# Performance work log

Measured on AMD Instinct MI355X. Metric: run time of the kernel, lower is better.

The kernel has to match this reference:

```python
import jax, jax.numpy as jnp
import numpy as np

EPS = 1e-5

def setup_inputs() -> dict:
    key = jax.random.key(0)
    ks = jax.random.split(key, 8)
    B, T, D, S = 8, 4096, 1024, 64
    return {
        "x": jax.random.normal(ks[0], (B, T, D), dtype=jnp.float32),
        "time_decay": jax.random.normal(ks[1], (S,), dtype=jnp.float32) * 0.1 - 0.5,
        "time_first": jax.random.normal(ks[2], (S,), dtype=jnp.float32) * 0.1,
        "W_key": jax.random.normal(ks[3], (S, D), dtype=jnp.float32) * 0.02,
        "W_value": jax.random.normal(ks[4], (S, D), dtype=jnp.float32) * 0.02,
        "W_output": jax.random.normal(ks[5], (D, S), dtype=jnp.float32) * 0.02,
        "W_shift": jax.random.normal(ks[6], (D, D), dtype=jnp.float32) * 0.02,
        "shift_gate": jnp.ones((D,), dtype=jnp.float32),
        "ln_w": jnp.ones((D,), dtype=jnp.float32),
        "ln_b": jnp.zeros((D,), dtype=jnp.float32),
    }


def _forward(x, time_decay, time_first, W_key, W_value, W_output, W_shift, shift_gate, ln_w, ln_b):
    B, T, D = x.shape
    S = time_decay.shape[0]
    # --- token shift: rotate sequence by shift_len, project, gated blend ---
    shift_len = max(1, int(T * 0.5))
    x_cat = jnp.concatenate([x[:, shift_len:], x[:, :-shift_len]], axis=1)  # (B,T,D)
    gate = jax.nn.sigmoid(shift_gate)
    x_shift = jnp.einsum('btd,ed->bte', x_cat, W_shift) * gate + x * (1.0 - gate)
    # --- layernorm (torch: biased variance, eps=1e-5) ---
    mu = jnp.mean(x_shift, axis=-1, keepdims=True)
    var = jnp.mean(jnp.square(x_shift - mu), axis=-1, keepdims=True)
    xn = (x_shift - mu) * jax.lax.rsqrt(var + EPS) * ln_w + ln_b
    # --- key/value projections and per-step wkv (fully vectorized) ---
    k = jnp.einsum('btd,sd->bts', xn, W_key)    # (B,T,S)
    v = jnp.einsum('btd,sd->bts', xn, W_value)  # (B,T,S)
    wkv = jnp.exp(-jnp.exp(time_first) * jax.nn.sigmoid(k)) * v  # (B,T,S)
    # --- linear recurrence: state = state*w + wkv_t, scanned over T ---
    w = jnp.exp(time_decay)  # (S,)
    def step(state, wkv_t):
        state = state * w + wkv_t
        return state, state
    init = jnp.zeros((B, S), dtype=x.dtype)
    last_state, states = jax.lax.scan(step, init, jnp.swapaxes(wkv, 0, 1))  # states: (T,B,S)
    states = jnp.swapaxes(states, 0, 1)  # (B,T,S)
    # --- batched output projection (applied per-step in torch; same math) ---
    output = jnp.einsum('bts,ds->btd', states, W_output)  # (B,T,D)
    return output, last_state


def reference(x, time_decay, time_first, W_key, W_value, W_output, W_shift, shift_gate, ln_w, ln_b):
    out, last_state = _forward(x, time_decay, time_first, W_key, W_value, W_output, W_shift, shift_gate, ln_w, ln_b)
    return out, jax.lax.stop_gradient(last_state)
```

## Files before the change

kernel.cpp:

```cpp
#include <hip/hip_runtime.h>
#include <stdint.h>

#define B_ 8
#define T_ 4096
#define D_ 1024
#define S_ 64
#define N_ 32768
#define OUT_ELEMS 33554432
#define NCHK 128
#define CHKL 32

typedef __attribute__((ext_vector_type(8))) short bf16x8;
typedef __attribute__((ext_vector_type(8))) unsigned short u16x8;
typedef __attribute__((ext_vector_type(4))) float f32x4;

__device__ __forceinline__ uint16_t f2bf(float f) {
    union { float f; uint32_t u; } v; v.f = f;
    uint32_t r = v.u + 0x7FFFu + ((v.u >> 16) & 1u);
    return (uint16_t)(r >> 16);
}
__device__ __forceinline__ float bf2f(uint16_t h) {
    union { uint32_t u; float f; } v; v.u = ((uint32_t)h) << 16;
    return v.f;
}

#define GLOAD_LDS16(gp, lp)                                             \
    __builtin_amdgcn_global_load_lds(                                   \
        (const __attribute__((address_space(1))) void*)(gp),            \
        (__attribute__((address_space(3))) void*)(lp), 16, 0, 0)

__global__ void cast_f32_bf16(const float* __restrict__ src,
                              uint16_t* __restrict__ dst, int n4) {
    int i = blockIdx.x * blockDim.x + threadIdx.x;
    if (i >= n4) return;
    float4 v = ((const float4*)src)[i];
    ushort4 o;
    o.x = f2bf(v.x); o.y = f2bf(v.y); o.z = f2bf(v.z); o.w = f2bf(v.w);
    ((ushort4*)dst)[i] = o;
}

__global__ void wprep(const float* __restrict__ Wsf, const float* __restrict__ Wkf,
                      const float* __restrict__ Wvf, const float* __restrict__ Wof,
                      const float* __restrict__ sg, const float* __restrict__ tf,
                      uint16_t* __restrict__ Wsb, uint16_t* __restrict__ Wkvb,
                      uint16_t* __restrict__ Wob, float* __restrict__ gbuf,
                      float* __restrict__ efirst)
{
    int i = blockIdx.x * blockDim.x + threadIdx.x;
    const float* src; uint16_t* dst; int j;
    if (i < 262144) { src = Wsf; dst = Wsb; j = i; }
    else if (i < 278528) { src = Wkf; dst = Wkvb; j = i - 262144; }
    else if (i < 294912) { src = Wvf; dst = Wkvb + 65536; j = i - 278528; }
    else if (i < 311296) { src = Wof; dst = Wob; j = i - 294912; }
    else if (i < 311552) {
        j = i - 311296;
        float4 v = ((const float4*)sg)[j];
        float4 g;
        g.x = 1.f / (1.f + __expf(-v.x)); g.y = 1.f / (1.f + __expf(-v.y));
        g.z = 1.f / (1.f + __expf(-v.z)); g.w = 1.f / (1.f + __expf(-v.w));
        ((float4*)gbuf)[j] = g;
        return;
    } else if (i < 311568) {
        j = i - 311552;
        float4 v = ((const float4*)tf)[j];
        float4 e;
        e.x = __expf(v.x); e.y = __expf(v.y); e.z = __expf(v.z); e.w = __expf(v.w);
        ((float4*)efirst)[j] = e;
        return;
    } else return;
    float4 v = ((const float4*)src)[j];
    ushort4 o;
    o.x = f2bf(v.x); o.y = f2bf(v.y); o.z = f2bf(v.z); o.w = f2bf(v.w);
    ((ushort4*)dst)[j] = o;
}

__global__ __launch_bounds__(256) void k1_shift_gemm(
    const uint16_t* __restrict__ xb, const uint16_t* __restrict__ Wsb,
    const float* __restrict__ gbuf, uint16_t* __restrict__ xs)
{
    __shared__ char sh[34816];
    uint16_t (*As)[64] = (uint16_t(*)[64])sh;
    uint16_t (*Bs)[64] = (uint16_t(*)[64])(sh + 16384);
    float (*epi)[68] = (float(*)[68])sh;

    const int tid = threadIdx.x;
    const int w = tid >> 6, lane = tid & 63, quad = lane >> 4, l16 = lane & 15;
    const int wm = w >> 1, wn = w & 1;
    const int lin = blockIdx.x;
    const int mt = (lin & 7) * 32 + (lin >> 6);
    const int nt = (lin >> 3) & 7;
    const int m0 = mt * 128, n0 = nt * 128;
    const int m0x = m0 ^ 2048;

    const int srow = w * 32 + (lane >> 3);
    const int scg  = ((lane & 7) ^ ((lane >> 3) & 7)) * 8;
    const uint16_t* aG = xb  + (size_t)(m0x + srow) * D_ + scg;
    const uint16_t* bG = Wsb + (size_t)(n0  + srow) * D_ + scg;

    f32x4 acc[4][4];
#pragma unroll
    for (int i = 0; i < 4; ++i)
#pragma unroll
        for (int j = 0; j < 4; ++j) acc[i][j] = (f32x4){0.f, 0.f, 0.f, 0.f};

    for (int k0 = 0; k0 < D_; k0 += 64) {
        __syncthreads();
#pragma unroll
        for (int i = 0; i < 4; ++i) {
            GLOAD_LDS16(aG + k0 + (size_t)(i * 8) * D_, &As[w * 32 + i * 8][0]);
            GLOAD_LDS16(bG + k0 + (size_t)(i * 8) * D_, &Bs[w * 32 + i * 8][0]);
        }
        __syncthreads();
#pragma unroll
        for (int ks = 0; ks < 2; ++ks) {
            bf16x8 a[4], b[4];
#pragma unroll
            for (int i = 0; i < 4; ++i)
                a[i] = *(const bf16x8*)&As[wm * 64 + i * 16 + l16]
                                         [(((ks * 4 + quad) ^ (l16 & 7)) * 8)];
#pragma unroll
            for (int j = 0; j < 4; ++j)
                b[j] = *(const bf16x8*)&Bs[wn * 64 + j * 16 + l16]
                                         [(((ks * 4 + quad) ^ (l16 & 7)) * 8)];
#pragma unroll
            for (int i = 0; i < 4; ++i)
#pragma unroll
                for (int j = 0; j < 4; ++j)
                    acc[i][j] = __builtin_amdgcn_mfma_f32_16x16x32_bf16(
                        a[i], b[j], acc[i][j], 0, 0, 0);
        }
    }

    const int row = tid >> 1;
    const int c0 = (tid & 1) * 32;
#pragma unroll
    for (int h = 0; h < 2; ++h) {
        __syncthreads();
        if (wn == h) {
#pragma unroll
            for (int i = 0; i < 4; ++i)
#pragma unroll
                for (int j = 0; j < 4; ++j)
#pragma unroll
                    for (int r = 0; r < 4; ++r)
                        epi[wm * 64 + i * 16 + quad * 4 + r][j * 16 + l16] =
                            acc[i][j][r];
        }
        __syncthreads();
        const int col = n0 + h * 64 + c0;
        const uint16_t* xrow = xb + (size_t)(m0 + row) * D_ + col;
        uint16_t* orow = xs + (size_t)(m0 + row) * D_ + col;
#pragma unroll
        for (int c4 = 0; c4 < 8; ++c4) {
            float4 g4 = ((const float4*)(gbuf + col))[c4];
            ushort4 xh = ((const ushort4*)xrow)[c4];
            const float* e = &epi[row][c0 + c4 * 4];
            ushort4 o;
            o.x = f2bf(e[0] * g4.x + bf2f(xh.x) * (1.f - g4.x));
            o.y = f2bf(e[1] * g4.y + bf2f(xh.y) * (1.f - g4.y));
            o.z = f2bf(e[2] * g4.z + bf2f(xh.z) * (1.f - g4.z));
            o.w = f2bf(e[3] * g4.w + bf2f(xh.w) * (1.f - g4.w));
            ((ushort4*)orow)[c4] = o;
        }
    }
}

__global__ __launch_bounds__(256) void k2_ln(uint16_t* __restrict__ xs,
                                             const float* __restrict__ ln_w,
                                             const float* __restrict__ ln_b)
{
    const int w = threadIdx.x >> 6, lane = threadIdx.x & 63;
    const size_t row = (size_t)blockIdx.x * 4 + w;
    uint16_t* p = xs + row * D_ + lane * 16;

    u16x8 h0 = *(const u16x8*)p;
    u16x8 h1 = *(const u16x8*)(p + 8);
    float v[16];
#pragma unroll
    for (int i = 0; i < 8; ++i) { v[i] = bf2f(h0[i]); v[8 + i] = bf2f(h1[i]); }
    float s = 0.f, q = 0.f;
#pragma unroll
    for (int i = 0; i < 16; ++i) { s += v[i]; q += v[i] * v[i]; }
#pragma unroll
    for (int off = 32; off > 0; off >>= 1) {
        s += __shfl_xor(s, off);
        q += __shfl_xor(q, off);
    }
    float mu = s * (1.f / D_);
    float var = q * (1.f / D_) - mu * mu;
    float rstd = rsqrtf(var + 1e-5f);

    const float* lw = ln_w + lane * 16;
    const float* lb = ln_b + lane * 16;
    u16x8 o0, o1;
#pragma unroll
    for (int i = 0; i < 8; ++i) {
        o0[i] = f2bf((v[i] - mu) * rstd * lw[i] + lb[i]);
        o1[i] = f2bf((v[8 + i] - mu) * rstd * lw[8 + i] + lb[8 + i]);
    }
    *(u16x8*)p = o0;
    *(u16x8*)(p + 8) = o1;
}

__global__ __launch_bounds__(256) void k3_kv(
    const uint16_t* __restrict__ xn, const uint16_t* __restrict__ Wkvb,
    const float* __restrict__ efirst, float* __restrict__ wkv)
{
    __shared__ char sh[33792];
    uint16_t (*As)[64] = (uint16_t(*)[64])sh;
    uint16_t (*Bs)[64] = (uint16_t(*)[64])(sh + 8192);
    float (*epi)[132] = (float(*)[132])sh;

    const int tid = threadIdx.x;
    const int w = tid >> 6, lane = tid & 63, quad = lane >> 4, l16 = lane & 15;
    const int wm = w >> 1, wn = w & 1;
    const int m0 = blockIdx.x * 64;

    const int lrow = w * 8 + (lane >> 3);
    const int scg  = ((lane & 7) ^ ((lane >> 3) & 7)) * 8;
    const uint16_t* aG = xn + (size_t)(m0 + lrow) * D_ + scg;
    const uint16_t* bG = Wkvb + (size_t)lrow * D_ + scg;

    f32x4 acc[2][4];
#pragma unroll
    for (int i = 0; i < 2; ++i)
#pragma unroll
        for (int j = 0; j < 4; ++j) acc[i][j] = (f32x4){0.f, 0.f, 0.f, 0.f};

    for (int k0 = 0; k0 < D_; k0 += 64) {
        __syncthreads();
#pragma unroll
        for (int i = 0; i < 2; ++i)
            GLOAD_LDS16(aG + k0 + (size_t)(i * 32) * D_, &As[lrow - (lane >> 3) + i * 32][0]);
#pragma unroll
        for (int i = 0; i < 4; ++i)
            GLOAD_LDS16(bG + k0 + (size_t)(i * 32) * D_, &Bs[lrow - (lane >> 3) + i * 32][0]);
        __syncthreads();
#pragma unroll
        for (int ks = 0; ks < 2; ++ks) {
            bf16x8 a[2], b[4];
#pragma unroll
            for (int i = 0; i < 2; ++i)
                a[i] = *(const bf16x8*)&As[wm * 32 + i * 16 + l16]
                                         [(((ks * 4 + quad) ^ (l16 & 7)) * 8)];
#pragma unroll
            for (int j = 0; j < 4; ++j)
                b[j] = *(const bf16x8*)&Bs[wn * 64 + j * 16 + l16]
                                         [(((ks * 4 + quad) ^ (l16 & 7)) * 8)];
#pragma unroll
            for (int i = 0; i < 2; ++i)
#pragma unroll
                for (int j = 0; j < 4; ++j)
                    acc[i][j] = __builtin_amdgcn_mfma_f32_16x16x32_bf16(
                        a[i], b[j], acc[i][j], 0, 0, 0);
        }
    }

    __syncthreads();
#pragma unroll
    for (int i = 0; i < 2; ++i)
#pragma unroll
        for (int j = 0; j < 4; ++j)
#pragma unroll
            for (int r = 0; r < 4; ++r)
                epi[wm * 32 + i * 16 + quad * 4 + r][wn * 64 + j * 16 + l16] =
                    acc[i][j][r];
    __syncthreads();

    const int row = tid >> 2, s0 = (tid & 3) * 16;
    float* dst = wkv + (size_t)(m0 + row) * S_ + s0;
#pragma unroll
    for (int c4 = 0; c4 < 4; ++c4) {
        float4 kk = *(const float4*)&epi[row][s0 + c4 * 4];
        float4 vv = *(const float4*)&epi[row][64 + s0 + c4 * 4];
        float4 ef = ((const float4*)(efirst + s0))[c4];
        float4 o;
        o.x = __expf(-ef.x / (1.f + __expf(-kk.x))) * vv.x;
        o.y = __expf(-ef.y / (1.f + __expf(-kk.y))) * vv.y;
        o.z = __expf(-ef.z / (1.f + __expf(-kk.z))) * vv.z;
        o.w = __expf(-ef.w / (1.f + __expf(-kk.w))) * vv.w;
        *(float4*)(dst + c4 * 4) = o;
    }
}

__global__ void k4a(const float* __restrict__ wkv,
                    const float* __restrict__ time_decay,
                    float* __restrict__ part)
{
    const int s = threadIdx.x;
    const int bc = blockIdx.x;
    const int b = bc >> 7, c = bc & (NCHK - 1);
    float w = expf(time_decay[s]);
    const float* src = wkv + ((size_t)b * T_ + c * CHKL) * S_ + s;
    float st = 0.f;
    for (int t = 0; t < CHKL; ++t) st = st * w + src[(size_t)t * S_];
    part[(size_t)bc * S_ + s] = st;
}
__global__ void k4b(const float* __restrict__ part,
                    const float* __restrict__ time_decay,
                    float* __restrict__ carry)
{
    const int s = threadIdx.x;
    const int b = blockIdx.x;
    float wL = expf(time_decay[s] * (float)CHKL);
    float cin = 0.f;
    for (int c = 0; c < NCHK; ++c) {
        size_t idx = ((size_t)b * NCHK + c) * S_ + s;
        carry[idx] = cin;
        cin = cin * wL + part[idx];
    }
}
__global__ void k4c(const float* __restrict__ wkv,
                    const float* __restrict__ time_decay,
                    const float* __restrict__ carry,
                    uint16_t* __restrict__ stb,
                    float* __restrict__ last_state)
{
    const int s = threadIdx.x;
    const int bc = blockIdx.x;
    const int b = bc >> 7, c = bc & (NCHK - 1);
    float w = expf(time_decay[s]);
    const float* src = wkv + ((size_t)b * T_ + c * CHKL) * S_ + s;
    uint16_t* dst = stb + ((size_t)b * T_ + c * CHKL) * S_ + s;
    float st = carry[(size_t)bc * S_ + s];
    for (int t = 0; t < CHKL; ++t) {
        st = st * w + src[(size_t)t * S_];
        dst[(size_t)t * S_] = f2bf(st);
    }
    if (c == NCHK - 1) last_state[b * S_ + s] = st;
}

__global__ __launch_bounds__(256) void k5_out(
    const uint16_t* __restrict__ st, const uint16_t* __restrict__ Wob,
    float* __restrict__ out)
{
    __shared__ float epi[128][68];
    const int tid = threadIdx.x;
    const int w = tid >> 6, lane = tid & 63, quad = lane >> 4, l16 = lane & 15;
    const int wm = w >> 1, wn = w & 1;
    const int m0b = blockIdx.y * 128;
    const int n0b = blockIdx.x * 128;

    f32x4 acc[4][4];
#pragma unroll
    for (int i = 0; i < 4; ++i)
#pragma unroll
        for (int j = 0; j < 4; ++j) acc[i][j] = (f32x4){0.f, 0.f, 0.f, 0.f};

#pragma unroll
    for (int k = 0; k < S_; k += 32) {
        bf16x8 a[4], b[4];
#pragma unroll
        for (int i = 0; i < 4; ++i)
            a[i] = *(const bf16x8*)(st + (size_t)(m0b + wm * 64 + i * 16 + l16) * S_ + k + quad * 8);
#pragma unroll
        for (int i = 0; i < 4; ++i)
            b[i] = *(const bf16x8*)(Wob + (size_t)(n0b + wn * 64 + i * 16 + l16) * S_ + k + quad * 8);
#pragma unroll
        for (int i = 0; i < 4; ++i)
#pragma unroll
            for (int j = 0; j < 4; ++j)
                acc[i][j] = __builtin_amdgcn_mfma_f32_16x16x32_bf16(
                    a[i], b[j], acc[i][j], 0, 0, 0);
    }

    const int row = tid >> 1;
    const int c0 = (tid & 1) * 32;
#pragma unroll
    for (int h = 0; h < 2; ++h) {
        __syncthreads();
        if (wn == h) {
#pragma unroll
            for (int i = 0; i < 4; ++i)
#pragma unroll
                for (int j = 0; j < 4; ++j)
#pragma unroll
                    for (int r = 0; r < 4; ++r)
                        epi[wm * 64 + i * 16 + quad * 4 + r][j * 16 + l16] =
                            acc[i][j][r];
        }
        __syncthreads();
        float* dst = out + (size_t)(m0b + row) * D_ + n0b + h * 64 + c0;
#pragma unroll
        for (int c4 = 0; c4 < 8; ++c4)
            ((float4*)dst)[c4] = *(const float4*)&epi[row][c0 + c4 * 4];
    }
}

extern "C" void kernel_launch(void* const* d_in, const int* in_sizes, int n_in,
                              void* d_out, int out_size, void* d_ws, size_t ws_size,
                              hipStream_t stream) {
    const float* x          = (const float*)d_in[0];
    const float* time_decay = (const float*)d_in[1];
    const float* time_first = (const float*)d_in[2];
    const float* W_key      = (const float*)d_in[3];
    const float* W_value    = (const float*)d_in[4];
    const float* W_output   = (const float*)d_in[5];
    const float* W_shift    = (const float*)d_in[6];
    const float* shift_gate = (const float*)d_in[7];
    const float* ln_w       = (const float*)d_in[8];
    const float* ln_b       = (const float*)d_in[9];
    float* out = (float*)d_out;

    char* ws = (char*)d_ws;
    uint16_t* xb    = (uint16_t*)(ws + 0);
    uint16_t* xs    = (uint16_t*)(ws + 67108864);
    float*    wkv   = (float*)   (ws + 134217728);
    uint16_t* stb   = (uint16_t*)(ws + 142606336);
    uint16_t* Wsb   = (uint16_t*)(ws + 146800640);
    uint16_t* Wkvb  = (uint16_t*)(ws + 148897792);
    uint16_t* Wob   = (uint16_t*)(ws + 149159936);
    float*    part  = (float*)   (ws + 149291008);
    float*    carry = (float*)   (ws + 149553152);
    float*    gbuf  = (float*)   (ws + 149815296);
    float*    efirst= (float*)   (ws + 149819392);

    cast_f32_bf16<<<32768, 256, 0, stream>>>(x, xb, OUT_ELEMS / 4);
    wprep<<<1218, 256, 0, stream>>>(W_shift, W_key, W_value, W_output,
                                    shift_gate, time_first,
                                    Wsb, Wkvb, Wob, gbuf, efirst);

    k1_shift_gemm<<<2048, 256, 0, stream>>>(xb, Wsb, gbuf, xs);
    k2_ln<<<N_ / 4, 256, 0, stream>>>(xs, ln_w, ln_b);
    k3_kv<<<512, 256, 0, stream>>>(xs, Wkvb, efirst, wkv);
    k4a<<<B_ * NCHK, S_, 0, stream>>>(wkv, time_decay, part);
    k4b<<<B_, S_, 0, stream>>>(part, time_decay, carry);
    k4c<<<B_ * NCHK, S_, 0, stream>>>(wkv, time_decay, carry, stb, out + OUT_ELEMS);
    k5_out<<<dim3(8, 256), 256, 0, stream>>>(stb, Wob, out);
}
```

Baseline: 434.5 us.

## Fold layernorm into KV GEMM epilogue via row stats; merge prep and scan kernels

Removes the standalone layernorm pass. The shift-GEMM epilogue accumulates per-row sum and sum-of-squares with atomics, ln_w is folded into the K/V weights, and the KV GEMM epilogue applies mean/rstd corrections using precomputed W·ln_w and W·ln_b vectors. This saves a full read-modify-write of the 64MB bf16 activation. The x cast and weight prep are merged into one launch, and the carry-scan kernel is folded into the final scan, with each chunk recomputing its prefix carry. Risks are atomic contention, worse accuracy from the E[x²]−μ² variance computed on unrounded values, and redundant prefix work in k4bc.

```diff
diff --git a/kernel.cpp b/kernel.cpp
--- a/kernel.cpp
+++ b/kernel.cpp
@@ -29,54 +29,86 @@
         (const __attribute__((address_space(1))) void*)(gp),            \
         (__attribute__((address_space(3))) void*)(lp), 16, 0, 0)
 
-__global__ void cast_f32_bf16(const float* __restrict__ src,
-                              uint16_t* __restrict__ dst, int n4) {
-    int i = blockIdx.x * blockDim.x + threadIdx.x;
-    if (i >= n4) return;
-    float4 v = ((const float4*)src)[i];
-    ushort4 o;
-    o.x = f2bf(v.x); o.y = f2bf(v.y); o.z = f2bf(v.z); o.w = f2bf(v.w);
-    ((ushort4*)dst)[i] = o;
-}
-
-__global__ void wprep(const float* __restrict__ Wsf, const float* __restrict__ Wkf,
-                      const float* __restrict__ Wvf, const float* __restrict__ Wof,
-                      const float* __restrict__ sg, const float* __restrict__ tf,
-                      uint16_t* __restrict__ Wsb, uint16_t* __restrict__ Wkvb,
-                      uint16_t* __restrict__ Wob, float* __restrict__ gbuf,
-                      float* __restrict__ efirst)
-{
-    int i = blockIdx.x * blockDim.x + threadIdx.x;
-    const float* src; uint16_t* dst; int j;
-    if (i < 262144) { src = Wsf; dst = Wsb; j = i; }
-    else if (i < 278528) { src = Wkf; dst = Wkvb; j = i - 262144; }
-    else if (i < 294912) { src = Wvf; dst = Wkvb + 65536; j = i - 278528; }
-    else if (i < 311296) { src = Wof; dst = Wob; j = i - 294912; }
-    else if (i < 311552) {
-        j = i - 311296;
-        float4 v = ((const float4*)sg)[j];
-        float4 g;
-        g.x = 1.f / (1.f + __expf(-v.x)); g.y = 1.f / (1.f + __expf(-v.y));
-        g.z = 1.f / (1.f + __expf(-v.z)); g.w = 1.f / (1.f + __expf(-v.w));
-        ((float4*)gbuf)[j] = g;
+__global__ void prep(const float* __restrict__ x,
+                     const float* __restrict__ Wsf, const float* __restrict__ Wkf,
+                     const float* __restrict__ Wvf, const float* __restrict__ Wof,
+                     const float* __restrict__ sg, const float* __restrict__ tf,
+                     const float* __restrict__ lnw, const float* __restrict__ lnb,
+                     uint16_t* __restrict__ xb, uint16_t* __restrict__ Wsb,
+                     uint16_t* __restrict__ Wkvb, uint16_t* __restrict__ Wob,
+                     float* __restrict__ gbuf, float* __restrict__ efirst,
+                     float* __restrict__ ucvec, float* __restrict__ rowstats)
+{
+    __shared__ float red[4];
+    const int blk = blockIdx.x, tid = threadIdx.x;
+    if (blk < 2048) {
+        for (int i = blk * 256 + tid; i < OUT_ELEMS / 4; i += 2048 * 256) {
+            float4 v = ((const float4*)x)[i];
+            ushort4 o;
+            o.x = f2bf(v.x); o.y = f2bf(v.y); o.z = f2bf(v.z); o.w = f2bf(v.w);
+            ((ushort4*)xb)[i] = o;
+        }
         return;
-    } else if (i < 311568) {
-        j = i - 311552;
-        float4 v = ((const float4*)tf)[j];
-        float4 e;
-        e.x = __expf(v.x); e.y = __expf(v.y); e.z = __expf(v.z); e.w = __expf(v.w);
-        ((float4*)efirst)[j] = e;
+    }
+    if (blk < 3298) {
+        int i = (blk - 2048) * 256 + tid;
+        const float* src; uint16_t* dst; int j; bool fold = false;
+        if (i < 262144) { src = Wsf; dst = Wsb; j = i; }
+        else if (i < 278528) { src = Wkf; dst = Wkvb; j = i - 262144; fold = true; }
+        else if (i < 294912) { src = Wvf; dst = Wkvb + 65536; j = i - 278528; fold = true; }
+        else if (i < 311296) { src = Wof; dst = Wob; j = i - 294912; }
+        else if (i < 311552) {
+            j = i - 311296;
+            float4 v = ((const float4*)sg)[j];
+            float4 g;
+            g.x = 1.f / (1.f + __expf(-v.x)); g.y = 1.f / (1.f + __expf(-v.y));
+            g.z = 1.f / (1.f + __expf(-v.z)); g.w = 1.f / (1.f + __expf(-v.w));
+            ((float4*)gbuf)[j] = g;
+            return;
+        } else if (i < 311568) {
+            j = i - 311552;
+            float4 v = ((const float4*)tf)[j];
+            float4 e;
+            e.x = __expf(v.x); e.y = __expf(v.y); e.z = __expf(v.z); e.w = __expf(v.w);
+            ((float4*)efirst)[j] = e;
+            return;
+        } else return;
+        float4 v = ((const float4*)src)[j];
+        if (fold) {
+            float4 l = ((const float4*)lnw)[j & 255];
+            v.x *= l.x; v.y *= l.y; v.z *= l.z; v.w *= l.w;
+        }
+        ushort4 o;
+        o.x = f2bf(v.x); o.y = f2bf(v.y); o.z = f2bf(v.z); o.w = f2bf(v.w);
+        ((ushort4*)dst)[j] = o;
         return;
-    } else return;
-    float4 v = ((const float4*)src)[j];
-    ushort4 o;
-    o.x = f2bf(v.x); o.y = f2bf(v.y); o.z = f2bf(v.z); o.w = f2bf(v.w);
-    ((ushort4*)dst)[j] = o;
+    }
+    if (blk < 3554) {
+        int b2 = blk - 3298;
+        int which = b2 >> 6, s = b2 & 63;
+        const float* W = (which < 2) ? Wkf : Wvf;
+        const float* L = (which & 1) ? lnb : lnw;
+        float4 wv = ((const float4*)W)[s * 256 + tid];
+        float4 lv = ((const float4*)L)[tid];
+        float p = wv.x * lv.x + wv.y * lv.y + wv.z * lv.z + wv.w * lv.w;
+#pragma unroll
+        for (int off = 32; off; off >>= 1) p += __shfl_xor(p, off);
+        if ((tid & 63) == 0) red[tid >> 6] = p;
+        __syncthreads();
+        if (tid == 0) ucvec[which * 64 + s] = red[0] + red[1] + red[2] + red[3];
+        return;
+    }
+    {
+        int i = (blk - 3554) * 256 + tid;
+        float4 z; z.x = 0.f; z.y = 0.f; z.z = 0.f; z.w = 0.f;
+        ((float4*)rowstats)[i] = z;
+    }
 }
 
 __global__ __launch_bounds__(256) void k1_shift_gemm(
     const uint16_t* __restrict__ xb, const uint16_t* __restrict__ Wsb,
-    const float* __restrict__ gbuf, uint16_t* __restrict__ xs)
+    const float* __restrict__ gbuf, uint16_t* __restrict__ xs,
+    float* __restrict__ rowstats)
 {
     __shared__ char sh[34816];
     uint16_t (*As)[64] = (uint16_t(*)[64])sh;
@@ -150,61 +182,36 @@
         const int col = n0 + h * 64 + c0;
         const uint16_t* xrow = xb + (size_t)(m0 + row) * D_ + col;
         uint16_t* orow = xs + (size_t)(m0 + row) * D_ + col;
+        float sr = 0.f, qr = 0.f;
 #pragma unroll
         for (int c4 = 0; c4 < 8; ++c4) {
             float4 g4 = ((const float4*)(gbuf + col))[c4];
             ushort4 xh = ((const ushort4*)xrow)[c4];
             const float* e = &epi[row][c0 + c4 * 4];
+            float b0 = e[0] * g4.x + bf2f(xh.x) * (1.f - g4.x);
+            float b1 = e[1] * g4.y + bf2f(xh.y) * (1.f - g4.y);
+            float b2 = e[2] * g4.z + bf2f(xh.z) * (1.f - g4.z);
+            float b3 = e[3] * g4.w + bf2f(xh.w) * (1.f - g4.w);
             ushort4 o;
-            o.x = f2bf(e[0] * g4.x + bf2f(xh.x) * (1.f - g4.x));
-            o.y = f2bf(e[1] * g4.y + bf2f(xh.y) * (1.f - g4.y));
-            o.z = f2bf(e[2] * g4.z + bf2f(xh.z) * (1.f - g4.z));
-            o.w = f2bf(e[3] * g4.w + bf2f(xh.w) * (1.f - g4.w));
+            o.x = f2bf(b0); o.y = f2bf(b1); o.z = f2bf(b2); o.w = f2bf(b3);
             ((ushort4*)orow)[c4] = o;
-        }
-    }
-}
-
-__global__ __launch_bounds__(256) void k2_ln(uint16_t* __restrict__ xs,
-                                             const float* __restrict__ ln_w,
-                                             const float* __restrict__ ln_b)
-{
-    const int w = threadIdx.x >> 6, lane = threadIdx.x & 63;
-    const size_t row = (size_t)blockIdx.x * 4 + w;
-    uint16_t* p = xs + row * D_ + lane * 16;
-
-    u16x8 h0 = *(const u16x8*)p;
-    u16x8 h1 = *(const u16x8*)(p + 8);
-    float v[16];
-#pragma unroll
-    for (int i = 0; i < 8; ++i) { v[i] = bf2f(h0[i]); v[8 + i] = bf2f(h1[i]); }
-    float s = 0.f, q = 0.f;
-#pragma unroll
-    for (int i = 0; i < 16; ++i) { s += v[i]; q += v[i] * v[i]; }
-#pragma unroll
-    for (int off = 32; off > 0; off >>= 1) {
-        s += __shfl_xor(s, off);
-        q += __shfl_xor(q, off);
-    }
-    float mu = s * (1.f / D_);
-    float var = q * (1.f / D_) - mu * mu;
-    float rstd = rsqrtf(var + 1e-5f);
-
-    const float* lw = ln_w + lane * 16;
-    const float* lb = ln_b + lane * 16;
-    u16x8 o0, o1;
-#pragma unroll
-    for (int i = 0; i < 8; ++i) {
-        o0[i] = f2bf((v[i] - mu) * rstd * lw[i] + lb[i]);
-        o1[i] = f2bf((v[8 + i] - mu) * rstd * lw[8 + i] + lb[8 + i]);
-    }
-    *(u16x8*)p = o0;
-    *(u16x8*)(p + 8) = o1;
+            sr += (b0 + b1) + (b2 + b3);
+            qr += (b0 * b0 + b1 * b1) + (b2 * b2 + b3 * b3);
+        }
+        sr += __shfl_xor(sr, 1);
+        qr += __shfl_xor(qr, 1);
+        if ((lane & 1) == 0) {
+            float* rs = rowstats + (size_t)(m0 + row) * 2;
+            atomicAdd(rs, sr);
+            atomicAdd(rs + 1, qr);
+        }
+    }
 }
 
 __global__ __launch_bounds__(256) void k3_kv(
-    const uint16_t* __restrict__ xn, const uint16_t* __restrict__ Wkvb,
-    const float* __restrict__ efirst, float* __restrict__ wkv)
+    const uint16_t* __restrict__ xsb, const uint16_t* __restrict__ Wkvb,
+    const float* __restrict__ efirst, const float* __restrict__ rowstats,
+    const float* __restrict__ ucvec, float* __restrict__ wkv)
 {
     __shared__ char sh[33792];
     uint16_t (*As)[64] = (uint16_t(*)[64])sh;
@@ -218,7 +225,7 @@
 
     const int lrow = w * 8 + (lane >> 3);
     const int scg  = ((lane & 7) ^ ((lane >> 3) & 7)) * 8;
-    const uint16_t* aG = xn + (size_t)(m0 + lrow) * D_ + scg;
+    const uint16_t* aG = xsb + (size_t)(m0 + lrow) * D_ + scg;
     const uint16_t* bG = Wkvb + (size_t)lrow * D_ + scg;
 
     f32x4 acc[2][4];
@@ -231,10 +238,10 @@
         __syncthreads();
 #pragma unroll
         for (int i = 0; i < 2; ++i)
-            GLOAD_LDS16(aG + k0 + (size_t)(i * 32) * D_, &As[lrow - (lane >> 3) + i * 32][0]);
+            GLOAD_LDS16(aG + k0 + (size_t)(i * 32) * D_, &As[w * 8 + i * 32][0]);
 #pragma unroll
         for (int i = 0; i < 4; ++i)
-            GLOAD_LDS16(bG + k0 + (size_t)(i * 32) * D_, &Bs[lrow - (lane >> 3) + i * 32][0]);
+            GLOAD_LDS16(bG + k0 + (size_t)(i * 32) * D_, &Bs[w * 8 + i * 32][0]);
         __syncthreads();
 #pragma unroll
         for (int ks = 0; ks < 2; ++ks) {
@@ -268,17 +275,33 @@
     __syncthreads();
 
     const int row = tid >> 2, s0 = (tid & 3) * 16;
+    const float2 rs = ((const float2*)rowstats)[m0 + row];
+    const float mu = rs.x * (1.f / (float)D_);
+    const float var = rs.y * (1.f / (float)D_) - mu * mu;
+    const float rstd = rsqrtf(var + 1e-5f);
     float* dst = wkv + (size_t)(m0 + row) * S_ + s0;
 #pragma unroll
     for (int c4 = 0; c4 < 4; ++c4) {
         float4 kk = *(const float4*)&epi[row][s0 + c4 * 4];
         float4 vv = *(const float4*)&epi[row][64 + s0 + c4 * 4];
+        float4 uk4 = *(const float4*)(ucvec + 0 * 64 + s0 + c4 * 4);
+        float4 ck4 = *(const float4*)(ucvec + 1 * 64 + s0 + c4 * 4);
+        float4 uv4 = *(const float4*)(ucvec + 2 * 64 + s0 + c4 * 4);
+        float4 cv4 = *(const float4*)(ucvec + 3 * 64 + s0 + c4 * 4);
         float4 ef = ((const float4*)(efirst + s0))[c4];
+        float kx = rstd * (kk.x - mu * uk4.x) + ck4.x;
+        float ky = rstd * (kk.y - mu * uk4.y) + ck4.y;
+        float kz = rstd * (kk.z - mu * uk4.z) + ck4.z;
+        float kw = rstd * (kk.w - mu * uk4.w) + ck4.w;
+        float vx = rstd * (vv.x - mu * uv4.x) + cv4.x;
+        float vy = rstd * (vv.y - mu * uv4.y) + cv4.y;
+        float vz = rstd * (vv.z - mu * uv4.z) + cv4.z;
+        float vw = rstd * (vv.w - mu * uv4.w) + cv4.w;
         float4 o;
-        o.x = __expf(-ef.x / (1.f + __expf(-kk.x))) * vv.x;
-        o.y = __expf(-ef.y / (1.f + __expf(-kk.y))) * vv.y;
-        o.z = __expf(-ef.z / (1.f + __expf(-kk.z))) * vv.z;
-        o.w = __expf(-ef.w / (1.f + __expf(-kk.w))) * vv.w;
+        o.x = __expf(-ef.x / (1.f + __expf(-kx))) * vx;
+        o.y = __expf(-ef.y / (1.f + __expf(-ky))) * vy;
+        o.z = __expf(-ef.z / (1.f + __expf(-kz))) * vz;
+        o.w = __expf(-ef.w / (1.f + __expf(-kw))) * vw;
         *(float4*)(dst + c4 * 4) = o;
     }
 }
@@ -293,36 +316,30 @@
     float w = expf(time_decay[s]);
     const float* src = wkv + ((size_t)b * T_ + c * CHKL) * S_ + s;
     float st = 0.f;
+#pragma unroll
     for (int t = 0; t < CHKL; ++t) st = st * w + src[(size_t)t * S_];
     part[(size_t)bc * S_ + s] = st;
 }
-__global__ void k4b(const float* __restrict__ part,
-                    const float* __restrict__ time_decay,
-                    float* __restrict__ carry)
-{
-    const int s = threadIdx.x;
-    const int b = blockIdx.x;
-    float wL = expf(time_decay[s] * (float)CHKL);
-    float cin = 0.f;
-    for (int c = 0; c < NCHK; ++c) {
-        size_t idx = ((size_t)b * NCHK + c) * S_ + s;
-        carry[idx] = cin;
-        cin = cin * wL + part[idx];
-    }
-}
-__global__ void k4c(const float* __restrict__ wkv,
-                    const float* __restrict__ time_decay,
-                    const float* __restrict__ carry,
-                    uint16_t* __restrict__ stb,
-                    float* __restrict__ last_state)
+__global__ void k4bc(const float* __restrict__ wkv,
+                     const float* __restrict__ time_decay,
+                     const float* __restrict__ part,
+                     uint16_t* __restrict__ stb,
+                     float* __restrict__ last_state)
 {
     const int s = threadIdx.x;
     const int bc = blockIdx.x;
     const int b = bc >> 7, c = bc & (NCHK - 1);
-    float w = expf(time_decay[s]);
+    const float td = time_decay[s];
+    const float w = expf(td);
+    const float wL = expf(td * (float)CHKL);
+    const float* pp = part + (size_t)b * NCHK * S_ + s;
+    float cin = 0.f;
+#pragma unroll 4
+    for (int j = 0; j < c; ++j) cin = cin * wL + pp[(size_t)j * S_];
     const float* src = wkv + ((size_t)b * T_ + c * CHKL) * S_ + s;
     uint16_t* dst = stb + ((size_t)b * T_ + c * CHKL) * S_ + s;
-    float st = carry[(size_t)bc * S_ + s];
+    float st = cin;
+#pragma unroll
     for (int t = 0; t < CHKL; ++t) {
         st = st * w + src[(size_t)t * S_];
         dst[(size_t)t * S_] = f2bf(st);
@@ -403,28 +420,26 @@
     float* out = (float*)d_out;
 
     char* ws = (char*)d_ws;
-    uint16_t* xb    = (uint16_t*)(ws + 0);
-    uint16_t* xs    = (uint16_t*)(ws + 67108864);
-    float*    wkv   = (float*)   (ws + 134217728);
-    uint16_t* stb   = (uint16_t*)(ws + 142606336);
-    uint16_t* Wsb   = (uint16_t*)(ws + 146800640);
-    uint16_t* Wkvb  = (uint16_t*)(ws + 148897792);
-    uint16_t* Wob   = (uint16_t*)(ws + 149159936);
-    float*    part  = (float*)   (ws + 149291008);
-    float*    carry = (float*)   (ws + 149553152);
-    float*    gbuf  = (float*)   (ws + 149815296);
-    float*    efirst= (float*)   (ws + 149819392);
-
-    cast_f32_bf16<<<32768, 256, 0, stream>>>(x, xb, OUT_ELEMS / 4);
-    wprep<<<1218, 256, 0, stream>>>(W_shift, W_key, W_value, W_output,
-                                    shift_gate, time_first,
-                                    Wsb, Wkvb, Wob, gbuf, efirst);
-
-    k1_shift_gemm<<<2048, 256, 0, stream>>>(xb, Wsb, gbuf, xs);
-    k2_ln<<<N_ / 4, 256, 0, stream>>>(xs, ln_w, ln_b);
-    k3_kv<<<512, 256, 0, stream>>>(xs, Wkvb, efirst, wkv);
+    uint16_t* xb      = (uint16_t*)(ws + 0);
+    uint16_t* xs      = (uint16_t*)(ws + 67108864);
+    float*    wkv     = (float*)   (ws + 134217728);
+    uint16_t* stb     = (uint16_t*)(ws + 142606336);
+    uint16_t* Wsb     = (uint16_t*)(ws + 146800640);
+    uint16_t* Wkvb    = (uint16_t*)(ws + 148897792);
+    uint16_t* Wob     = (uint16_t*)(ws + 149159936);
+    float*    part    = (float*)   (ws + 149291008);
+    float*    rowstats= (float*)   (ws + 149553152);
+    float*    gbuf    = (float*)   (ws + 149815296);
+    float*    efirst  = (float*)   (ws + 149819392);
+    float*    ucvec   = (float*)   (ws + 149819648);
+
+    prep<<<3618, 256, 0, stream>>>(x, W_shift, W_key, W_value, W_output,
+                                   shift_gate, time_first, ln_w, ln_b,
+                                   xb, Wsb, Wkvb, Wob, gbuf, efirst,
+                                   ucvec, rowstats);
+    k1_shift_gemm<<<2048, 256, 0, stream>>>(xb, Wsb, gbuf, xs, rowstats);
+    k3_kv<<<512, 256, 0, stream>>>(xs, Wkvb, efirst, rowstats, ucvec, wkv);
     k4a<<<B_ * NCHK, S_, 0, stream>>>(wkv, time_decay, part);
-    k4b<<<B_, S_, 0, stream>>>(part, time_decay, carry);
-    k4c<<<B_ * NCHK, S_, 0, stream>>>(wkv, time_decay, carry, stb, out + OUT_ELEMS);
+    k4bc<<<B_ * NCHK, S_, 0, stream>>>(wkv, time_decay, part, stb, out + OUT_ELEMS);
     k5_out<<<dim3(8, 256), 256, 0, stream>>>(stb, Wob, out);
 }
```

Measured after the change: 429.0 us. About the same (-1.3%).
